# Performance work log

Measured on AMD Instinct MI355X. Metric: run time of the kernel, lower is better.

The kernel has to match this reference:

```python
import jax, jax.numpy as jnp
import numpy as np

QUERY_DIM, KEY_DIM, N_BATCH, N_KEYS = 512, 256, 2048, 512

def setup_inputs() -> dict:
    key = jax.random.key(0)
    k1, k2, k3, k4, k5, k6 = jax.random.split(key, 6)
    queries = jax.random.normal(k1, (N_BATCH, QUERY_DIM), dtype=jnp.float32)
    keys = jax.random.normal(k2, (N_BATCH, N_KEYS, KEY_DIM), dtype=jnp.float32)
    trans_keys = jax.random.normal(k3, (N_BATCH, N_KEYS, KEY_DIM), dtype=jnp.float32)
    null_mask = jax.random.randint(k4, (N_BATCH, N_KEYS), 0, 2).astype(jnp.bool_)
    # nn.Linear(query_dim, key_dim) params
    bound = 1.0 / np.sqrt(QUERY_DIM)
    W = jax.random.uniform(k5, (KEY_DIM, QUERY_DIM), dtype=jnp.float32, minval=-bound, maxval=bound)
    b = jax.random.uniform(k6, (KEY_DIM,), dtype=jnp.float32, minval=-bound, maxval=bound)
    return {"queries": queries, "keys": keys, "trans_keys": trans_keys,
            "null_mask": null_mask, "W": W, "b": b}

def reference(queries, keys, trans_keys, null_mask, W, b):
    # trans_queries = linear_in(queries): (B, key_dim)
    trans_queries = queries @ W.T + b
    # alpha = bmm(keys, trans_queries[:, :, None]).squeeze(2): (B, n_keys)
    alpha = jnp.einsum('bnk,bk->bn', keys, trans_queries)
    alpha = jnp.where(null_mask, -jnp.inf, alpha)
    alpha_sm = jax.nn.softmax(alpha, axis=1)
    # attened_keys = bmm(alpha_sm[:, None, :], keys).squeeze(1): (B, key_dim)
    attened_keys = jnp.einsum('bn,bnk->bk', alpha_sm, keys)
    return (attened_keys, alpha_sm)
```

## Files before the change

kernel.cpp:

```cpp
#include <hip/hip_runtime.h>
#include <stdint.h>

#define QD 512
#define KD 256
#define NBATCH 2048
#define NK 512

__global__ __launch_bounds__(256) void tq_gemm(const float* __restrict__ Q,
                                               const float* __restrict__ W,
                                               const float* __restrict__ bias,
                                               float* __restrict__ TQ,
                                               int* __restrict__ flag) {
    if (blockIdx.x == 0 && threadIdx.x == 0) *flag = 0;

    __shared__ float qs[4][QD];
    const int b0 = blockIdx.x * 4;

    const float4* Qv = (const float4*)(Q + (size_t)b0 * QD);
    float4* qsv = (float4*)&qs[0][0];
    qsv[threadIdx.x]       = Qv[threadIdx.x];
    qsv[threadIdx.x + 256] = Qv[threadIdx.x + 256];
    __syncthreads();

    const int k = threadIdx.x;
    const float4* Wv = (const float4*)(W + (size_t)k * QD);

    float a0 = 0.f, a1 = 0.f, a2 = 0.f, a3 = 0.f;
#pragma unroll 4
    for (int kk = 0; kk < QD / 4; ++kk) {
        float4 w4 = Wv[kk];
        float4 q0 = *(const float4*)&qs[0][kk * 4];
        float4 q1 = *(const float4*)&qs[1][kk * 4];
        float4 q2 = *(const float4*)&qs[2][kk * 4];
        float4 q3 = *(const float4*)&qs[3][kk * 4];
        a0 += w4.x * q0.x + w4.y * q0.y + w4.z * q0.z + w4.w * q0.w;
        a1 += w4.x * q1.x + w4.y * q1.y + w4.z * q1.z + w4.w * q1.w;
        a2 += w4.x * q2.x + w4.y * q2.y + w4.z * q2.z + w4.w * q2.w;
        a3 += w4.x * q3.x + w4.y * q3.y + w4.z * q3.z + w4.w * q3.w;
    }
    const float bb = bias[k];
    TQ[(size_t)(b0 + 0) * KD + k] = a0 + bb;
    TQ[(size_t)(b0 + 1) * KD + k] = a1 + bb;
    TQ[(size_t)(b0 + 2) * KD + k] = a2 + bb;
    TQ[(size_t)(b0 + 3) * KD + k] = a3 + bb;
}

__global__ __launch_bounds__(256) void detect_mask_dtype(const uint32_t* __restrict__ m,
                                                         int nwords,
                                                         int* __restrict__ flag) {
    uint32_t v = 0;
    for (int i = blockIdx.x * blockDim.x + threadIdx.x; i < nwords;
         i += gridDim.x * blockDim.x)
        v |= m[i];
#pragma unroll
    for (int off = 32; off > 0; off >>= 1)
        v |= (uint32_t)__shfl_xor((int)v, off, 64);
    if ((threadIdx.x & 63) == 0 && v > 1u) atomicOr(flag, 1);
}

__global__ __launch_bounds__(256) void attn_fused(const float* __restrict__ keys,
                                                  const void* __restrict__ maskp,
                                                  const float* __restrict__ TQ,
                                                  const int* __restrict__ flag,
                                                  float* __restrict__ out_att,
                                                  float* __restrict__ out_alpha) {
    const int b    = blockIdx.x;
    const int wave = threadIdx.x >> 6;
    const int lane = threadIdx.x & 63;

    __shared__ float s_alpha[NK];
    __shared__ float s_acc[4][KD];
    __shared__ float s_m[4], s_l[4];

    const int bytemask = *flag;

    const float4 tq4 = *(const float4*)(TQ + (size_t)b * KD + lane * 4);
    const float* kb  = keys + (size_t)b * NK * KD;
    const uint8_t* mb8  = (const uint8_t*)maskp + (size_t)b * NK;
    const int32_t* mb32 = (const int32_t*)maskp + (size_t)b * NK;

    float m = -1e30f, l = 0.f;
    float ax = 0.f, ay = 0.f, az = 0.f, aw = 0.f;

    const int n0 = wave * (NK / 4);

    for (int i = 0; i < NK / 4; i += 4) {
        float4 k4[4];
#pragma unroll
        for (int r = 0; r < 4; ++r)
            k4[r] = *(const float4*)(kb + (size_t)(n0 + i + r) * KD + lane * 4);

#pragma unroll
        for (int r = 0; r < 4; ++r) {
            const int n = n0 + i + r;
            float part = k4[r].x * tq4.x + k4[r].y * tq4.y +
                         k4[r].z * tq4.z + k4[r].w * tq4.w;
#pragma unroll
            for (int off = 32; off > 0; off >>= 1)
                part += __shfl_xor(part, off, 64);

            const int masked = bytemask ? (mb8[n] != 0) : (mb32[n] != 0);
            const float aval = masked ? -INFINITY : part;
            if (lane == 0) s_alpha[n] = aval;

            const float mn = fmaxf(m, aval);
            const float sc = __expf(m - mn);
            const float w  = __expf(aval - mn);
            l = l * sc + w;
            ax = ax * sc + w * k4[r].x;
            ay = ay * sc + w * k4[r].y;
            az = az * sc + w * k4[r].z;
            aw = aw * sc + w * k4[r].w;
            m = mn;
        }
    }

    if (lane == 0) { s_m[wave] = m; s_l[wave] = l; }
    *(float4*)&s_acc[wave][lane * 4] = make_float4(ax, ay, az, aw);
    __syncthreads();

    const float M = fmaxf(fmaxf(s_m[0], s_m[1]), fmaxf(s_m[2], s_m[3]));
    const float sc0 = __expf(s_m[0] - M), sc1 = __expf(s_m[1] - M);
    const float sc2 = __expf(s_m[2] - M), sc3 = __expf(s_m[3] - M);
    const float L = s_l[0] * sc0 + s_l[1] * sc1 + s_l[2] * sc2 + s_l[3] * sc3;
    const float invL = 1.0f / L;

    const int t = threadIdx.x;
    const float o = (s_acc[0][t] * sc0 + s_acc[1][t] * sc1 +
                     s_acc[2][t] * sc2 + s_acc[3][t] * sc3) * invL;
    out_att[(size_t)b * KD + t] = o;

    out_alpha[(size_t)b * NK + t]       = __expf(s_alpha[t]       - M) * invL;
    out_alpha[(size_t)b * NK + t + 256] = __expf(s_alpha[t + 256] - M) * invL;
}

extern "C" void kernel_launch(void* const* d_in, const int* in_sizes, int n_in,
                              void* d_out, int out_size, void* d_ws, size_t ws_size,
                              hipStream_t stream) {
    const float* queries = (const float*)d_in[0];
    const float* keys    = (const float*)d_in[1];
    const void*  mask    = d_in[3];
    const float* W       = (const float*)d_in[4];
    const float* bias    = (const float*)d_in[5];

    float* out_att   = (float*)d_out;
    float* out_alpha = (float*)d_out + (size_t)NBATCH * KD;
    float* TQ        = (float*)d_ws;
    int*   flag      = (int*)((char*)d_ws + (size_t)NBATCH * KD * sizeof(float));

    const int mask_words = in_sizes[3] / 4;

    tq_gemm<<<NBATCH / 4, 256, 0, stream>>>(queries, W, bias, TQ, flag);
    detect_mask_dtype<<<256, 256, 0, stream>>>((const uint32_t*)mask, mask_words, flag);
    attn_fused<<<NBATCH, 256, 0, stream>>>(keys, mask, TQ, flag, out_att, out_alpha);
}
```

Baseline: 244.1 us.

## Fold mask dtype detection into attention kernel and unroll key loop deeper

Drops the separate mask-dtype detection kernel and its global flag. Each attention block now inspects its own mask row, builds a shared-memory additive bias of 0 or -inf, and replaces per-key mask loads with shared reads. The key loop also loads 8 rows per iteration instead of 4, and the online-softmax rescale runs only when the running max grows. This removes a launch and a full pass over the mask, but with a byte mask the per-block word read can run past the end of the mask buffer, and detection now depends on each row's contents.

```diff
diff --git a/kernel.cpp b/kernel.cpp
--- a/kernel.cpp
+++ b/kernel.cpp
@@ -9,10 +9,7 @@
 __global__ __launch_bounds__(256) void tq_gemm(const float* __restrict__ Q,
                                                const float* __restrict__ W,
                                                const float* __restrict__ bias,
-                                               float* __restrict__ TQ,
-                                               int* __restrict__ flag) {
-    if (blockIdx.x == 0 && threadIdx.x == 0) *flag = 0;
-
+                                               float* __restrict__ TQ) {
     __shared__ float qs[4][QD];
     const int b0 = blockIdx.x * 4;
 
@@ -45,73 +42,79 @@
     TQ[(size_t)(b0 + 3) * KD + k] = a3 + bb;
 }
 
-__global__ __launch_bounds__(256) void detect_mask_dtype(const uint32_t* __restrict__ m,
-                                                         int nwords,
-                                                         int* __restrict__ flag) {
-    uint32_t v = 0;
-    for (int i = blockIdx.x * blockDim.x + threadIdx.x; i < nwords;
-         i += gridDim.x * blockDim.x)
-        v |= m[i];
-#pragma unroll
-    for (int off = 32; off > 0; off >>= 1)
-        v |= (uint32_t)__shfl_xor((int)v, off, 64);
-    if ((threadIdx.x & 63) == 0 && v > 1u) atomicOr(flag, 1);
-}
-
 __global__ __launch_bounds__(256) void attn_fused(const float* __restrict__ keys,
                                                   const void* __restrict__ maskp,
                                                   const float* __restrict__ TQ,
-                                                  const int* __restrict__ flag,
                                                   float* __restrict__ out_att,
                                                   float* __restrict__ out_alpha) {
     const int b    = blockIdx.x;
-    const int wave = threadIdx.x >> 6;
-    const int lane = threadIdx.x & 63;
+    const int t    = threadIdx.x;
+    const int wave = t >> 6;
+    const int lane = t & 63;
 
+    __shared__ float s_bias[NK];
     __shared__ float s_alpha[NK];
     __shared__ float s_acc[4][KD];
     __shared__ float s_m[4], s_l[4];
+    __shared__ int   s_flag[4];
 
-    const int bytemask = *flag;
+    const uint32_t* mw32 = (const uint32_t*)maskp + (size_t)b * NK;
+    const uint32_t* mw8  = (const uint32_t*)((const uint8_t*)maskp + (size_t)b * NK);
+    uint2 wv = ((const uint2*)mw32)[t];
+    const bool big = (wv.x > 1u) | (wv.y > 1u);
+    const unsigned long long bal = __ballot(big);
+    if (lane == 0) s_flag[wave] = (bal != 0ull);
+    __syncthreads();
+    const int bytemask = s_flag[0] | s_flag[1] | s_flag[2] | s_flag[3];
+    if (bytemask) {
+        if (t < NK / 4) {
+            uint32_t w = mw8[t];
+            s_bias[4 * t + 0] = (w & 0x000000FFu) ? -INFINITY : 0.f;
+            s_bias[4 * t + 1] = (w & 0x0000FF00u) ? -INFINITY : 0.f;
+            s_bias[4 * t + 2] = (w & 0x00FF0000u) ? -INFINITY : 0.f;
+            s_bias[4 * t + 3] = (w & 0xFF000000u) ? -INFINITY : 0.f;
+        }
+    } else {
+        s_bias[2 * t + 0] = wv.x ? -INFINITY : 0.f;
+        s_bias[2 * t + 1] = wv.y ? -INFINITY : 0.f;
+    }
+    __syncthreads();
 
     const float4 tq4 = *(const float4*)(TQ + (size_t)b * KD + lane * 4);
     const float* kb  = keys + (size_t)b * NK * KD;
-    const uint8_t* mb8  = (const uint8_t*)maskp + (size_t)b * NK;
-    const int32_t* mb32 = (const int32_t*)maskp + (size_t)b * NK;
 
     float m = -1e30f, l = 0.f;
     float ax = 0.f, ay = 0.f, az = 0.f, aw = 0.f;
 
     const int n0 = wave * (NK / 4);
 
-    for (int i = 0; i < NK / 4; i += 4) {
-        float4 k4[4];
+    for (int i = 0; i < NK / 4; i += 8) {
+        float4 k4[8];
 #pragma unroll
-        for (int r = 0; r < 4; ++r)
+        for (int r = 0; r < 8; ++r)
             k4[r] = *(const float4*)(kb + (size_t)(n0 + i + r) * KD + lane * 4);
 
 #pragma unroll
-        for (int r = 0; r < 4; ++r) {
+        for (int r = 0; r < 8; ++r) {
             const int n = n0 + i + r;
-            float part = k4[r].x * tq4.x + k4[r].y * tq4.y +
-                         k4[r].z * tq4.z + k4[r].w * tq4.w;
+            float d = k4[r].x * tq4.x + k4[r].y * tq4.y +
+                      k4[r].z * tq4.z + k4[r].w * tq4.w;
 #pragma unroll
             for (int off = 32; off > 0; off >>= 1)
-                part += __shfl_xor(part, off, 64);
+                d += __shfl_xor(d, off, 64);
 
-            const int masked = bytemask ? (mb8[n] != 0) : (mb32[n] != 0);
-            const float aval = masked ? -INFINITY : part;
+            const float aval = d + s_bias[n];
             if (lane == 0) s_alpha[n] = aval;
 
-            const float mn = fmaxf(m, aval);
-            const float sc = __expf(m - mn);
-            const float w  = __expf(aval - mn);
-            l = l * sc + w;
-            ax = ax * sc + w * k4[r].x;
-            ay = ay * sc + w * k4[r].y;
-            az = az * sc + w * k4[r].z;
-            aw = aw * sc + w * k4[r].w;
-            m = mn;
+            if (aval > m) {
+                const float sc = __expf(m - aval);
+                l *= sc; ax *= sc; ay *= sc; az *= sc; aw *= sc;
+                m = aval;
+            }
+            const float w = __expf(aval - m);
+            l += w;
+            ax += w * k4[r].x; ay += w * k4[r].y;
+            az += w * k4[r].z; aw += w * k4[r].w;
         }
     }
 
@@ -125,7 +128,6 @@
     const float L = s_l[0] * sc0 + s_l[1] * sc1 + s_l[2] * sc2 + s_l[3] * sc3;
     const float invL = 1.0f / L;
 
-    const int t = threadIdx.x;
     const float o = (s_acc[0][t] * sc0 + s_acc[1][t] * sc1 +
                      s_acc[2][t] * sc2 + s_acc[3][t] * sc3) * invL;
     out_att[(size_t)b * KD + t] = o;
@@ -146,11 +148,7 @@
     float* out_att   = (float*)d_out;
     float* out_alpha = (float*)d_out + (size_t)NBATCH * KD;
     float* TQ        = (float*)d_ws;
-    int*   flag      = (int*)((char*)d_ws + (size_t)NBATCH * KD * sizeof(float));
 
-    const int mask_words = in_sizes[3] / 4;
-
-    tq_gemm<<<NBATCH / 4, 256, 0, stream>>>(queries, W, bias, TQ, flag);
-    detect_mask_dtype<<<256, 256, 0, stream>>>((const uint32_t*)mask, mask_words, flag);
-    attn_fused<<<NBATCH, 256, 0, stream>>>(keys, mask, TQ, flag, out_att, out_alpha);
+    tq_gemm<<<NBATCH / 4, 256, 0, stream>>>(queries, W, bias, TQ);
+    attn_fused<<<NBATCH, 256, 0, stream>>>(keys, mask, TQ, out_att, out_alpha);
 }
```

New measurement: 246.8 us. About the same (+1.1%).
